# Kernel tuning notes

Hardware: AMD Instinct MI355X
Metric: run time of the kernel (lower is better)

The kernel has to match this reference:

```python
import jax, jax.numpy as jnp
import numpy as np

EPS = 1e-5


def _pointwise_bn_relu(x, W, b, gamma, beta):
    # x: [B,N,Cin], W: [Cout,Cin] (kernel-1 Conv1d == pointwise linear)
    y = jnp.einsum('bnc,oc->bno', x, W) + b
    # BatchNorm1d over channel dim (stats over batch and points), train-mode stats
    mu = y.mean(axis=(0, 1))
    var = y.var(axis=(0, 1))
    y = (y - mu) * jax.lax.rsqrt(var + EPS) * gamma + beta
    return jax.nn.relu(y)


def setup_inputs() -> dict:
    key = jax.random.key(0)
    ks = jax.random.split(key, 8)
    B, N = 4, 16384
    C_img, C_lidar = 64, 64
    H, Wd = 16, 64
    img_size = H * Wd  # 1024
    d_in = C_img + C_lidar  # 128
    mlp1 = [128, 64]

    lidar_features = jax.random.normal(ks[0], (B, N, C_lidar), dtype=jnp.float32)
    img_features = jax.random.normal(ks[1], (B, C_img, H, Wd), dtype=jnp.float32)

    def lin(k, cout, cin):
        return jax.random.normal(k, (cout, cin), dtype=jnp.float32) / np.sqrt(cin)

    W1 = lin(ks[2], mlp1[0], d_in)
    b1 = jnp.zeros((mlp1[0],), jnp.float32)
    g1 = jnp.ones((mlp1[0],), jnp.float32)
    be1 = jnp.zeros((mlp1[0],), jnp.float32)
    W2 = lin(ks[3], mlp1[1], mlp1[0])
    b2 = jnp.zeros((mlp1[1],), jnp.float32)
    g2 = jnp.ones((mlp1[1],), jnp.float32)
    be2 = jnp.zeros((mlp1[1],), jnp.float32)
    W3 = lin(ks[4], img_size, mlp1[1])
    b3 = jnp.zeros((img_size,), jnp.float32)

    return dict(lidar_features=lidar_features, img_features=img_features,
                W1=W1, b1=b1, g1=g1, be1=be1,
                W2=W2, b2=b2, g2=g2, be2=be2,
                W3=W3, b3=b3)


def reference(lidar_features, img_features, W1, b1, g1, be1, W2, b2, g2, be2, W3, b3):
    B, N, _ = lidar_features.shape
    Bc, C, H, Wd = img_features.shape
    K = H * Wd  # img_size
    img_flat = img_features.reshape(B, C, K)  # [B,C,K]

    # global average pool over image, broadcast-concat with lidar features
    g = img_flat.mean(-1)  # [B,C]
    x = jnp.concatenate([jnp.broadcast_to(g[:, None, :], (B, N, C)), lidar_features], axis=-1)

    x = _pointwise_bn_relu(x, W1, b1, g1, be1)
    x = _pointwise_bn_relu(x, W2, b2, g2, be2)
    x = jnp.einsum('bnc,oc->bno', x, W3) + b3  # [B,N,K] mask logits, no BN/act

    # mean over img_size of broadcast multiply == batched GEMM (avoids [B,C,N,K] blow-up)
    out = jnp.einsum('bnk,bck->bnc', x, img_flat) / K  # [B,N,C]
    return out
```

## Files before the change

kernel.cpp:

```cpp
#include <hip/hip_runtime.h>
#include <math.h>

#define NROW   65536
#define INV_BN (1.f/65536.f)
#define EPSF   1e-5f
#define PAD1   132

__global__ __launch_bounds__(256) void k_prep(const float* __restrict__ img,
        const float* __restrict__ W3, const float* __restrict__ b3,
        float* __restrict__ g, float* __restrict__ MT, float* __restrict__ dv) {
    __shared__ float imgs[1024];
    __shared__ float mr[4][64];
    __shared__ float red[256];
    __shared__ float red2[256];
    const int bc = blockIdx.x;
    const int t = threadIdx.x;
    const int b = bc >> 6, c = bc & 63;
    for (int k = t; k < 1024; k += 256) imgs[k] = img[bc*1024 + k];
    __syncthreads();
    const int j = t & 63, kk = t >> 6;
    float a = 0.f;
    #pragma unroll 4
    for (int k = kk*256; k < kk*256 + 256; ++k) a += imgs[k] * W3[k*64 + j];
    mr[kk][j] = a;
    float d = 0.f, s = 0.f;
    #pragma unroll 4
    for (int k = t; k < 1024; k += 256) { d += b3[k]*imgs[k]; s += imgs[k]; }
    red[t] = d; red2[t] = s;
    __syncthreads();
    if (t < 64) MT[(b*64 + t)*64 + c] = (mr[0][t]+mr[1][t]+mr[2][t]+mr[3][t]) * (1.f/1024.f);
    for (int w = 128; w > 0; w >>= 1) {
        if (t < w) { red[t] += red[t+w]; red2[t] += red2[t+w]; }
        __syncthreads();
    }
    if (t == 0) { dv[bc] = red[0]*(1.f/1024.f); g[bc] = red2[0]*(1.f/1024.f); }
}

__global__ __launch_bounds__(512) void k_wt(const float* __restrict__ W1,
        const float* __restrict__ W2, const float* __restrict__ b1,
        const float* __restrict__ g, float* __restrict__ W1hT,
        float* __restrict__ W2T, float* __restrict__ c1) {
    const int t = threadIdx.x;
    for (int i = t; i < 8192; i += 512) {
        int c = i >> 7, o = i & 127;
        W1hT[i] = W1[o*128 + 64 + c];
    }
    for (int i = t; i < 8192; i += 512) {
        int o = i >> 6, jj = i & 63;
        W2T[i] = W2[jj*128 + o];
    }
    const int b = t >> 7, o = t & 127;
    float s = b1[o];
    #pragma unroll 8
    for (int c = 0; c < 64; ++c) s += g[b*64 + c] * W1[o*128 + c];
    c1[t] = s;
}

__global__ __launch_bounds__(256) void k_gemm1(const float* __restrict__ lidar,
        const float* __restrict__ W1hT, const float* __restrict__ c1,
        float* __restrict__ y1T, float* __restrict__ st) {
    __shared__ __align__(16) float Lt[64*PAD1];
    __shared__ __align__(16) float Ws[64*128];
    const int t = threadIdx.x;
    const int base = blockIdx.x * 128;
    const int b = base >> 14;
    {
        const int c = t & 63, r0 = (t >> 6) * 32;
        #pragma unroll 8
        for (int i = 0; i < 32; ++i)
            Lt[c*PAD1 + r0 + i] = lidar[(base + r0 + i)*64 + c];
    }
    for (int f = t; f < 2048; f += 256)
        *(float4*)&Ws[f*4] = *(const float4*)&W1hT[f*4];
    __syncthreads();

    const int rg = (t & 15) * 8, og = (t >> 4) * 8;
    float acc[8][8] = {};
    #pragma unroll 2
    for (int c = 0; c < 64; ++c) {
        float la[8], wa[8];
        *(float4*)&la[0] = *(const float4*)&Lt[c*PAD1 + rg];
        *(float4*)&la[4] = *(const float4*)&Lt[c*PAD1 + rg + 4];
        *(float4*)&wa[0] = *(const float4*)&Ws[c*128 + og];
        *(float4*)&wa[4] = *(const float4*)&Ws[c*128 + og + 4];
        #pragma unroll
        for (int ri = 0; ri < 8; ++ri)
            #pragma unroll
            for (int oi = 0; oi < 8; ++oi)
                acc[ri][oi] += la[ri] * wa[oi];
    }
    float cb[8];
    *(float4*)&cb[0] = *(const float4*)&c1[b*128 + og];
    *(float4*)&cb[4] = *(const float4*)&c1[b*128 + og + 4];
    float s[8] = {}, q[8] = {};
    #pragma unroll
    for (int ri = 0; ri < 8; ++ri)
        #pragma unroll
        for (int oi = 0; oi < 8; ++oi) {
            float v = acc[ri][oi] + cb[oi];
            acc[ri][oi] = v; s[oi] += v; q[oi] += v*v;
        }
    #pragma unroll
    for (int oi = 0; oi < 8; ++oi) {
        float4 v0 = {acc[0][oi],acc[1][oi],acc[2][oi],acc[3][oi]};
        float4 v1 = {acc[4][oi],acc[5][oi],acc[6][oi],acc[7][oi]};
        *(float4*)&y1T[(og+oi)*NROW + base + rg]     = v0;
        *(float4*)&y1T[(og+oi)*NROW + base + rg + 4] = v1;
    }
    __syncthreads();
    float* red = Lt;
    const int rgi = t & 15;
    #pragma unroll
    for (int oi = 0; oi < 8; ++oi) red[rgi*128 + og + oi] = s[oi];
    __syncthreads();
    if (t < 128) { float a = 0.f;
        #pragma unroll
        for (int k = 0; k < 16; ++k) a += red[k*128 + t];
        atomicAdd(&st[t], a); }
    __syncthreads();
    #pragma unroll
    for (int oi = 0; oi < 8; ++oi) red[rgi*128 + og + oi] = q[oi];
    __syncthreads();
    if (t < 128) { float a = 0.f;
        #pragma unroll
        for (int k = 0; k < 16; ++k) a += red[k*128 + t];
        atomicAdd(&st[128 + t], a); }
}

__global__ void k_fin1(const float* __restrict__ st, const float* __restrict__ g1,
                       const float* __restrict__ be1, float* __restrict__ sc) {
    const int o = threadIdx.x;
    float mu = st[o] * INV_BN;
    float var = st[128 + o] * INV_BN - mu*mu;
    float s = g1[o] * rsqrtf(var + EPSF);
    sc[o] = s; sc[128 + o] = be1[o] - mu*s;
}
__global__ void k_fin2(const float* __restrict__ st2, const float* __restrict__ g2,
                       const float* __restrict__ be2, float* __restrict__ sc2) {
    const int o = threadIdx.x;
    float mu = st2[o] * INV_BN;
    float var = st2[64 + o] * INV_BN - mu*mu;
    float s = g2[o] * rsqrtf(var + EPSF);
    sc2[o] = s; sc2[64 + o] = be2[o] - mu*s;
}

__global__ __launch_bounds__(256) void k_gemm2(const float* __restrict__ y1T,
        const float* __restrict__ W2T, const float* __restrict__ sc,
        const float* __restrict__ b2, float* __restrict__ y2T, float* __restrict__ st2) {
    __shared__ __align__(16) float Ys[128*64];
    __shared__ __align__(16) float Ws[128*64];
    const int t = threadIdx.x;
    const int base = blockIdx.x * 64;
    for (int f = t; f < 2048; f += 256) {
        int o = f >> 4, r4 = (f & 15) * 4;
        float4 v = *(const float4*)&y1T[o*NROW + base + r4];
        float scl = sc[o], sh = sc[128 + o];
        v.x = fmaxf(v.x*scl + sh, 0.f); v.y = fmaxf(v.y*scl + sh, 0.f);
        v.z = fmaxf(v.z*scl + sh, 0.f); v.w = fmaxf(v.w*scl + sh, 0.f);
        *(float4*)&Ys[o*64 + r4] = v;
    }
    for (int f = t; f < 2048; f += 256)
        *(float4*)&Ws[f*4] = *(const float4*)&W2T[f*4];
    __syncthreads();

    const int rg = (t & 15) * 4, jg = (t >> 4) * 4;
    float acc[4][4] = {};
    #pragma unroll 4
    for (int o = 0; o < 128; ++o) {
        float ya[4], wa[4];
        *(float4*)ya = *(const float4*)&Ys[o*64 + rg];
        *(float4*)wa = *(const float4*)&Ws[o*64 + jg];
        #pragma unroll
        for (int ri = 0; ri < 4; ++ri)
            #pragma unroll
            for (int ji = 0; ji < 4; ++ji)
                acc[ri][ji] += ya[ri] * wa[ji];
    }
    float bb[4]; *(float4*)bb = *(const float4*)&b2[jg];
    float s[4] = {}, q[4] = {};
    #pragma unroll
    for (int ri = 0; ri < 4; ++ri)
        #pragma unroll
        for (int ji = 0; ji < 4; ++ji) {
            float v = acc[ri][ji] + bb[ji];
            acc[ri][ji] = v; s[ji] += v; q[ji] += v*v;
        }
    #pragma unroll
    for (int ji = 0; ji < 4; ++ji) {
        float4 v = {acc[0][ji],acc[1][ji],acc[2][ji],acc[3][ji]};
        *(float4*)&y2T[(jg+ji)*NROW + base + rg] = v;
    }
    __syncthreads();
    float* red = Ys;
    #pragma unroll
    for (int ji = 0; ji < 4; ++ji) red[(t&15)*64 + jg + ji] = s[ji];
    __syncthreads();
    if (t < 64) { float a = 0.f;
        #pragma unroll
        for (int k = 0; k < 16; ++k) a += red[k*64 + t];
        atomicAdd(&st2[t], a); }
    __syncthreads();
    #pragma unroll
    for (int ji = 0; ji < 4; ++ji) red[(t&15)*64 + jg + ji] = q[ji];
    __syncthreads();
    if (t < 64) { float a = 0.f;
        #pragma unroll
        for (int k = 0; k < 16; ++k) a += red[k*64 + t];
        atomicAdd(&st2[64 + t], a); }
}

__global__ __launch_bounds__(256) void k_gemm3(const float* __restrict__ y2T,
        const float* __restrict__ MT, const float* __restrict__ dv,
        const float* __restrict__ sc2, float* __restrict__ out) {
    __shared__ __align__(16) float Ys[64*128];
    __shared__ __align__(16) float Ms[64*64];
    const int t = threadIdx.x;
    const int base = blockIdx.x * 128;
    const int b = base >> 14;
    for (int f = t; f < 2048; f += 256) {
        int j = f >> 5, r4 = (f & 31) * 4;
        float4 v = *(const float4*)&y2T[j*NROW + base + r4];
        float scl = sc2[j], sh = sc2[64 + j];
        v.x = fmaxf(v.x*scl + sh, 0.f); v.y = fmaxf(v.y*scl + sh, 0.f);
        v.z = fmaxf(v.z*scl + sh, 0.f); v.w = fmaxf(v.w*scl + sh, 0.f);
        *(float4*)&Ys[j*128 + r4] = v;
    }
    for (int f = t; f < 1024; f += 256)
        *(float4*)&Ms[f*4] = *(const float4*)&MT[b*4096 + f*4];
    __syncthreads();

    const int rg = (t & 15) * 8, cg = (t >> 4) * 4;
    float acc[8][4] = {};
    #pragma unroll 4
    for (int j = 0; j < 64; ++j) {
        float ya[8], ma[4];
        *(float4*)&ya[0] = *(const float4*)&Ys[j*128 + rg];
        *(float4*)&ya[4] = *(const float4*)&Ys[j*128 + rg + 4];
        *(float4*)ma = *(const float4*)&Ms[j*64 + cg];
        #pragma unroll
        for (int ri = 0; ri < 8; ++ri)
            #pragma unroll
            for (int ci = 0; ci < 4; ++ci)
                acc[ri][ci] += ya[ri] * ma[ci];
    }
    float db[4]; *(float4*)db = *(const float4*)&dv[b*64 + cg];
    #pragma unroll
    for (int ri = 0; ri < 8; ++ri) {
        float4 v = {acc[ri][0]+db[0], acc[ri][1]+db[1], acc[ri][2]+db[2], acc[ri][3]+db[3]};
        *(float4*)&out[(base + rg + ri)*64 + cg] = v;
    }
}

extern "C" void kernel_launch(void* const* d_in, const int* in_sizes, int n_in,
                              void* d_out, int out_size, void* d_ws, size_t ws_size,
                              hipStream_t stream) {
    const float* lidar = (const float*)d_in[0];
    const float* img   = (const float*)d_in[1];
    const float* W1  = (const float*)d_in[2];
    const float* b1  = (const float*)d_in[3];
    const float* g1  = (const float*)d_in[4];
    const float* be1 = (const float*)d_in[5];
    const float* W2  = (const float*)d_in[6];
    const float* b2  = (const float*)d_in[7];
    const float* g2  = (const float*)d_in[8];
    const float* be2 = (const float*)d_in[9];
    const float* W3  = (const float*)d_in[10];
    const float* b3  = (const float*)d_in[11];

    float* ws   = (float*)d_ws;
    float* y1T  = ws;
    float* y2T  = y1T + 128*NROW;
    float* g    = y2T + 64*NROW;
    float* c1   = g   + 256;
    float* MT   = c1  + 512;
    float* dv   = MT  + 16384;
    float* W1hT = dv  + 256;
    float* W2T  = W1hT + 8192;
    float* st   = W2T + 8192;
    float* sc   = st  + 384;

    hipMemsetAsync(st, 0, 384 * sizeof(float), stream);

    k_prep <<<256,  256, 0, stream>>>(img, W3, b3, g, MT, dv);
    k_wt   <<<1,    512, 0, stream>>>(W1, W2, b1, g, W1hT, W2T, c1);
    k_gemm1<<<512,  256, 0, stream>>>(lidar, W1hT, c1, y1T, st);
    k_fin1 <<<1,    128, 0, stream>>>(st, g1, be1, sc);
    k_gemm2<<<1024, 256, 0, stream>>>(y1T, W2T, sc, b2, y2T, st + 256);
    k_fin2 <<<1,    64,  0, stream>>>(st + 256, g2, be2, sc + 256);
    k_gemm3<<<512,  256, 0, stream>>>(y2T, MT, dv, sc + 256, (float*)d_out);
}
```

Before: 203.8 us.

## Replace register-tiled GEMMs with per-lane row kernels and separate BN stats kernels

Rewrites the three GEMM kernels so each thread owns one row and a slice of output channels, reading weights straight from global memory (wave-uniform broadcasts) instead of staging them in shared memory with 8x8 register tiles. Batch-norm statistics are no longer fused into the GEMM epilogues. Two new reduction kernels reread y1T and y2T to compute sums and squared sums. This removes the shared-memory weight staging and epilogue reductions, but adds two extra kernel launches and an extra full read of both intermediates. Each loaded activation is also reused across fewer outputs.

```diff
diff --git a/kernel.cpp b/kernel.cpp
--- a/kernel.cpp
+++ b/kernel.cpp
@@ -4,7 +4,6 @@
 #define NROW   65536
 #define INV_BN (1.f/65536.f)
 #define EPSF   1e-5f
-#define PAD1   132
 
 __global__ __launch_bounds__(256) void k_prep(const float* __restrict__ img,
         const float* __restrict__ W3, const float* __restrict__ b3,
@@ -58,73 +57,70 @@
 
 __global__ __launch_bounds__(256) void k_gemm1(const float* __restrict__ lidar,
         const float* __restrict__ W1hT, const float* __restrict__ c1,
-        float* __restrict__ y1T, float* __restrict__ st) {
-    __shared__ __align__(16) float Lt[64*PAD1];
-    __shared__ __align__(16) float Ws[64*128];
-    const int t = threadIdx.x;
-    const int base = blockIdx.x * 128;
+        float* __restrict__ y1T) {
+    __shared__ float Lt[64*65];
+    const int t = threadIdx.x;
+    const int base = blockIdx.x * 64;
     const int b = base >> 14;
-    {
-        const int c = t & 63, r0 = (t >> 6) * 32;
-        #pragma unroll 8
-        for (int i = 0; i < 32; ++i)
-            Lt[c*PAD1 + r0 + i] = lidar[(base + r0 + i)*64 + c];
-    }
-    for (int f = t; f < 2048; f += 256)
-        *(float4*)&Ws[f*4] = *(const float4*)&W1hT[f*4];
-    __syncthreads();
-
-    const int rg = (t & 15) * 8, og = (t >> 4) * 8;
-    float acc[8][8] = {};
+    const int lane = t & 63;
+    const int wo = (t >> 6) * 32;
+    for (int i = t; i < 4096; i += 256) {
+        int r = i >> 6, c = i & 63;
+        Lt[c*65 + r] = lidar[(base + r)*64 + c];
+    }
+    __syncthreads();
+    float acc[32] = {};
     #pragma unroll 2
     for (int c = 0; c < 64; ++c) {
-        float la[8], wa[8];
-        *(float4*)&la[0] = *(const float4*)&Lt[c*PAD1 + rg];
-        *(float4*)&la[4] = *(const float4*)&Lt[c*PAD1 + rg + 4];
-        *(float4*)&wa[0] = *(const float4*)&Ws[c*128 + og];
-        *(float4*)&wa[4] = *(const float4*)&Ws[c*128 + og + 4];
+        float a = Lt[c*65 + lane];
         #pragma unroll
-        for (int ri = 0; ri < 8; ++ri)
-            #pragma unroll
-            for (int oi = 0; oi < 8; ++oi)
-                acc[ri][oi] += la[ri] * wa[oi];
-    }
-    float cb[8];
-    *(float4*)&cb[0] = *(const float4*)&c1[b*128 + og];
-    *(float4*)&cb[4] = *(const float4*)&c1[b*128 + og + 4];
-    float s[8] = {}, q[8] = {};
+        for (int oi = 0; oi < 32; ++oi)
+            acc[oi] += a * W1hT[c*128 + wo + oi];
+    }
     #pragma unroll
-    for (int ri = 0; ri < 8; ++ri)
-        #pragma unroll
-        for (int oi = 0; oi < 8; ++oi) {
-            float v = acc[ri][oi] + cb[oi];
-            acc[ri][oi] = v; s[oi] += v; q[oi] += v*v;
-        }
-    #pragma unroll
-    for (int oi = 0; oi < 8; ++oi) {
-        float4 v0 = {acc[0][oi],acc[1][oi],acc[2][oi],acc[3][oi]};
-        float4 v1 = {acc[4][oi],acc[5][oi],acc[6][oi],acc[7][oi]};
-        *(float4*)&y1T[(og+oi)*NROW + base + rg]     = v0;
-        *(float4*)&y1T[(og+oi)*NROW + base + rg + 4] = v1;
-    }
-    __syncthreads();
-    float* red = Lt;
-    const int rgi = t & 15;
-    #pragma unroll
-    for (int oi = 0; oi < 8; ++oi) red[rgi*128 + og + oi] = s[oi];
-    __syncthreads();
-    if (t < 128) { float a = 0.f;
-        #pragma unroll
-        for (int k = 0; k < 16; ++k) a += red[k*128 + t];
-        atomicAdd(&st[t], a); }
-    __syncthreads();
-    #pragma unroll
-    for (int oi = 0; oi < 8; ++oi) red[rgi*128 + og + oi] = q[oi];
-    __syncthreads();
-    if (t < 128) { float a = 0.f;
-        #pragma unroll
-        for (int k = 0; k < 16; ++k) a += red[k*128 + t];
-        atomicAdd(&st[128 + t], a); }
+    for (int oi = 0; oi < 32; ++oi)
+        y1T[(wo + oi)*NROW + base + lane] = acc[oi] + c1[b*128 + wo + oi];
+}
+
+__global__ __launch_bounds__(256) void k_st1(const float* __restrict__ y1T, float* __restrict__ st) {
+    __shared__ float r1[256], r2[256];
+    const int t = threadIdx.x;
+    const int o = blockIdx.x >> 2;
+    const int q = blockIdx.x & 3;
+    const float4* p = (const float4*)(y1T + o*NROW + q*16384);
+    float s = 0.f, sq = 0.f;
+    #pragma unroll 4
+    for (int i = t; i < 4096; i += 256) {
+        float4 v = p[i];
+        s  += v.x + v.y + v.z + v.w;
+        sq += v.x*v.x + v.y*v.y + v.z*v.z + v.w*v.w;
+    }
+    r1[t] = s; r2[t] = sq; __syncthreads();
+    for (int w = 128; w > 0; w >>= 1) {
+        if (t < w) { r1[t] += r1[t+w]; r2[t] += r2[t+w]; }
+        __syncthreads();
+    }
+    if (t == 0) { atomicAdd(&st[o], r1[0]); atomicAdd(&st[128 + o], r2[0]); }
+}
+__global__ __launch_bounds__(256) void k_st2(const float* __restrict__ y2T, float* __restrict__ st2) {
+    __shared__ float r1[256], r2[256];
+    const int t = threadIdx.x;
+    const int o = blockIdx.x >> 3;
+    const int q = blockIdx.x & 7;
+    const float4* p = (const float4*)(y2T + o*NROW + q*8192);
+    float s = 0.f, sq = 0.f;
+    #pragma unroll 4
+    for (int i = t; i < 2048; i += 256) {
+        float4 v = p[i];
+        s  += v.x + v.y + v.z + v.w;
+        sq += v.x*v.x + v.y*v.y + v.z*v.z + v.w*v.w;
+    }
+    r1[t] = s; r2[t] = sq; __syncthreads();
+    for (int w = 128; w > 0; w >>= 1) {
+        if (t < w) { r1[t] += r1[t+w]; r2[t] += r2[t+w]; }
+        __syncthreads();
+    }
+    if (t == 0) { atomicAdd(&st2[o], r1[0]); atomicAdd(&st2[64 + o], r2[0]); }
 }
 
 __global__ void k_fin1(const float* __restrict__ st, const float* __restrict__ g1,
@@ -146,108 +142,50 @@
 
 __global__ __launch_bounds__(256) void k_gemm2(const float* __restrict__ y1T,
         const float* __restrict__ W2T, const float* __restrict__ sc,
-        const float* __restrict__ b2, float* __restrict__ y2T, float* __restrict__ st2) {
-    __shared__ __align__(16) float Ys[128*64];
-    __shared__ __align__(16) float Ws[128*64];
+        const float* __restrict__ b2, float* __restrict__ y2T) {
     const int t = threadIdx.x;
     const int base = blockIdx.x * 64;
-    for (int f = t; f < 2048; f += 256) {
-        int o = f >> 4, r4 = (f & 15) * 4;
-        float4 v = *(const float4*)&y1T[o*NROW + base + r4];
-        float scl = sc[o], sh = sc[128 + o];
-        v.x = fmaxf(v.x*scl + sh, 0.f); v.y = fmaxf(v.y*scl + sh, 0.f);
-        v.z = fmaxf(v.z*scl + sh, 0.f); v.w = fmaxf(v.w*scl + sh, 0.f);
-        *(float4*)&Ys[o*64 + r4] = v;
-    }
-    for (int f = t; f < 2048; f += 256)
-        *(float4*)&Ws[f*4] = *(const float4*)&W2T[f*4];
-    __syncthreads();
-
-    const int rg = (t & 15) * 4, jg = (t >> 4) * 4;
-    float acc[4][4] = {};
+    const int lane = t & 63;
+    const int wj = (t >> 6) * 16;
+    float acc[16] = {};
     #pragma unroll 4
     for (int o = 0; o < 128; ++o) {
-        float ya[4], wa[4];
-        *(float4*)ya = *(const float4*)&Ys[o*64 + rg];
-        *(float4*)wa = *(const float4*)&Ws[o*64 + jg];
+        float v = y1T[o*NROW + base + lane];
+        v = fmaxf(v * sc[o] + sc[128 + o], 0.f);
         #pragma unroll
-        for (int ri = 0; ri < 4; ++ri)
-            #pragma unroll
-            for (int ji = 0; ji < 4; ++ji)
-                acc[ri][ji] += ya[ri] * wa[ji];
-    }
-    float bb[4]; *(float4*)bb = *(const float4*)&b2[jg];
-    float s[4] = {}, q[4] = {};
+        for (int ji = 0; ji < 16; ++ji)
+            acc[ji] += v * W2T[o*64 + wj + ji];
+    }
     #pragma unroll
-    for (int ri = 0; ri < 4; ++ri)
-        #pragma unroll
-        for (int ji = 0; ji < 4; ++ji) {
-            float v = acc[ri][ji] + bb[ji];
-            acc[ri][ji] = v; s[ji] += v; q[ji] += v*v;
-        }
-    #pragma unroll
-    for (int ji = 0; ji < 4; ++ji) {
-        float4 v = {acc[0][ji],acc[1][ji],acc[2][ji],acc[3][ji]};
-        *(float4*)&y2T[(jg+ji)*NROW + base + rg] = v;
-    }
-    __syncthreads();
-    float* red = Ys;
-    #pragma unroll
-    for (int ji = 0; ji < 4; ++ji) red[(t&15)*64 + jg + ji] = s[ji];
-    __syncthreads();
-    if (t < 64) { float a = 0.f;
-        #pragma unroll
-        for (int k = 0; k < 16; ++k) a += red[k*64 + t];
-        atomicAdd(&st2[t], a); }
-    __syncthreads();
-    #pragma unroll
-    for (int ji = 0; ji < 4; ++ji) red[(t&15)*64 + jg + ji] = q[ji];
-    __syncthreads();
-    if (t < 64) { float a = 0.f;
-        #pragma unroll
-        for (int k = 0; k < 16; ++k) a += red[k*64 + t];
-        atomicAdd(&st2[64 + t], a); }
+    for (int ji = 0; ji < 16; ++ji)
+        y2T[(wj + ji)*NROW + base + lane] = acc[ji] + b2[wj + ji];
 }
 
 __global__ __launch_bounds__(256) void k_gemm3(const float* __restrict__ y2T,
         const float* __restrict__ MT, const float* __restrict__ dv,
         const float* __restrict__ sc2, float* __restrict__ out) {
-    __shared__ __align__(16) float Ys[64*128];
-    __shared__ __align__(16) float Ms[64*64];
-    const int t = threadIdx.x;
-    const int base = blockIdx.x * 128;
+    __shared__ float Ot[64*65];
+    const int t = threadIdx.x;
+    const int base = blockIdx.x * 64;
     const int b = base >> 14;
-    for (int f = t; f < 2048; f += 256) {
-        int j = f >> 5, r4 = (f & 31) * 4;
-        float4 v = *(const float4*)&y2T[j*NROW + base + r4];
-        float scl = sc2[j], sh = sc2[64 + j];
-        v.x = fmaxf(v.x*scl + sh, 0.f); v.y = fmaxf(v.y*scl + sh, 0.f);
-        v.z = fmaxf(v.z*scl + sh, 0.f); v.w = fmaxf(v.w*scl + sh, 0.f);
-        *(float4*)&Ys[j*128 + r4] = v;
-    }
-    for (int f = t; f < 1024; f += 256)
-        *(float4*)&Ms[f*4] = *(const float4*)&MT[b*4096 + f*4];
-    __syncthreads();
-
-    const int rg = (t & 15) * 8, cg = (t >> 4) * 4;
-    float acc[8][4] = {};
+    const int lane = t & 63;
+    const int wc = (t >> 6) * 16;
+    float acc[16] = {};
     #pragma unroll 4
     for (int j = 0; j < 64; ++j) {
-        float ya[8], ma[4];
-        *(float4*)&ya[0] = *(const float4*)&Ys[j*128 + rg];
-        *(float4*)&ya[4] = *(const float4*)&Ys[j*128 + rg + 4];
-        *(float4*)ma = *(const float4*)&Ms[j*64 + cg];
+        float v = y2T[j*NROW + base + lane];
+        v = fmaxf(v * sc2[j] + sc2[64 + j], 0.f);
         #pragma unroll
-        for (int ri = 0; ri < 8; ++ri)
-            #pragma unroll
-            for (int ci = 0; ci < 4; ++ci)
-                acc[ri][ci] += ya[ri] * ma[ci];
-    }
-    float db[4]; *(float4*)db = *(const float4*)&dv[b*64 + cg];
+        for (int ci = 0; ci < 16; ++ci)
+            acc[ci] += v * MT[(b*64 + j)*64 + wc + ci];
+    }
     #pragma unroll
-    for (int ri = 0; ri < 8; ++ri) {
-        float4 v = {acc[ri][0]+db[0], acc[ri][1]+db[1], acc[ri][2]+db[2], acc[ri][3]+db[3]};
-        *(float4*)&out[(base + rg + ri)*64 + cg] = v;
+    for (int ci = 0; ci < 16; ++ci)
+        Ot[(wc + ci)*65 + lane] = acc[ci] + dv[b*64 + wc + ci];
+    __syncthreads();
+    for (int i = t; i < 4096; i += 256) {
+        int r = i >> 6, c = i & 63;
+        out[(base + r)*64 + c] = Ot[c*65 + r];
     }
 }
 
@@ -283,9 +221,11 @@
 
     k_prep <<<256,  256, 0, stream>>>(img, W3, b3, g, MT, dv);
     k_wt   <<<1,    512, 0, stream>>>(W1, W2, b1, g, W1hT, W2T, c1);
-    k_gemm1<<<512,  256, 0, stream>>>(lidar, W1hT, c1, y1T, st);
+    k_gemm1<<<1024, 256, 0, stream>>>(lidar, W1hT, c1, y1T);
+    k_st1  <<<512,  256, 0, stream>>>(y1T, st);
     k_fin1 <<<1,    128, 0, stream>>>(st, g1, be1, sc);
-    k_gemm2<<<1024, 256, 0, stream>>>(y1T, W2T, sc, b2, y2T, st + 256);
+    k_gemm2<<<1024, 256, 0, stream>>>(y1T, W2T, sc, b2, y2T);
+    k_st2  <<<512,  256, 0, stream>>>(y2T, st + 256);
     k_fin2 <<<1,    64,  0, stream>>>(st + 256, g2, be2, sc + 256);
-    k_gemm3<<<512,  256, 0, stream>>>(y2T, MT, dv, sc + 256, (float*)d_out);
-}
+    k_gemm3<<<1024, 256, 0, stream>>>(y2T, MT, dv, sc + 256, (float*)d_out);
+}
```

Measured after the change: 310.7 us. +52.4%, slower.
